# Kernel tuning notes

Measured on AMD Instinct MI355X. Metric: run time of the kernel, lower is better.

Reference implementation:

```python
import jax, jax.numpy as jnp
import numpy as np

DK = 64

def setup_inputs() -> dict:
    key = jax.random.key(0)
    kx, kq, kk, kv = jax.random.split(key, 4)
    B, T, DM, DV = 256, 256, 384, 64
    x = jax.random.normal(kx, (B, T, DM), dtype=jnp.float32)
    s = 1.0 / np.sqrt(DM)
    W_q = jax.random.normal(kq, (DM, DK), dtype=jnp.float32) * s
    W_k = jax.random.normal(kk, (DM, DK), dtype=jnp.float32) * s
    W_v = jax.random.normal(kv, (DM, DV), dtype=jnp.float32) * s
    return {"x": x, "W_q": W_q, "W_k": W_k, "W_v": W_v}

def reference(x, W_q, W_k, W_v):
    # x: [B, T, dm]; projections to [B, T, dk]/[B, T, dv]
    q = jnp.einsum('btc,ck->btk', x, W_q)
    k = jnp.einsum('btc,ck->btk', x, W_k)
    v = jnp.einsum('btc,cv->btv', x, W_v)
    scale = k.shape[-1] ** (-0.5)
    wei = jnp.einsum('btk,bsk->bts', q, k) * scale  # [B, T, T]
    T = x.shape[1]
    causal = jnp.tril(jnp.ones((T, T), dtype=bool))
    wei = jnp.where(causal, wei, -jnp.inf)
    wei = jax.nn.softmax(wei, axis=-1)
    # dropout omitted (eval mode / deterministic reference)
    out = jnp.einsum('bts,bsv->btv', wei, v)
    return out
```

## Files before the change

kernel.cpp:

```cpp
#include <hip/hip_runtime.h>


typedef __attribute__((ext_vector_type(8))) short short8;
typedef __attribute__((ext_vector_type(4))) float floatx4;

__device__ inline unsigned short f2bf(float f) {
  union { float f; unsigned u; } v; v.f = f;
  unsigned r = v.u + 0x7FFFu + ((v.u >> 16) & 1u);
  return (unsigned short)(r >> 16);
}

__device__ inline void glds16(const void* g, void* l) {
  __builtin_amdgcn_global_load_lds(
      (const __attribute__((address_space(1))) void*)g,
      (__attribute__((address_space(3))) void*)l, 16, 0, 0);
}

__global__ void wt_kernel(const float* __restrict__ wq, const float* __restrict__ wk,
                          const float* __restrict__ wv, unsigned short* __restrict__ wt) {
  int idx = blockIdx.x * 256 + threadIdx.x;
  if (idx >= 3 * 64 * 384) return;
  int mat = idx / (64 * 384);
  int rem = idx % (64 * 384);
  int n = rem / 384, k = rem % 384;
  const float* w = (mat == 0) ? wq : ((mat == 1) ? wk : wv);
  wt[idx] = f2bf(w[k * 64 + n]);
}

__global__ __launch_bounds__(1024) void fused_kernel(
    const float* __restrict__ x, const unsigned short* __restrict__ wt,
    float* __restrict__ out) {
  __shared__ __align__(16) unsigned short wb[2][3 * 192 * 32];
  __shared__ __align__(16) unsigned short sK[256 * 72];
  __shared__ __align__(16) unsigned short sVT[64 * 264];

  int tid = threadIdx.x, lane = tid & 63, w = tid >> 6;
  int m = lane & 15, q = lane >> 4;
  int b = blockIdx.x;
  const float* xb = x + (size_t)b * 256 * 384;

  auto stage = [&](int mega, int buf) {
#pragma unroll
    for (int t = 0; t < 3; ++t) {
      int i = w + 16 * t;
      if (i < 36) {
        int kc = i / 12, sub = i % 12;
        int c = sub * 16 + (lane >> 2), g = lane & 3;
        glds16(wt + (size_t)c * 384 + (mega * 3 + kc) * 32 + g * 8,
               (void*)&wb[buf][kc * 6144 + sub * 512]);
      }
    }
  };

  floatx4 z = {0.f, 0.f, 0.f, 0.f};
  floatx4 acc[12];
#pragma unroll
  for (int nt = 0; nt < 12; ++nt) acc[nt] = z;

  stage(0, 0);
#pragma unroll
  for (int mega = 0; mega < 4; ++mega) {
    int buf = mega & 1;
    __syncthreads();
    if (mega < 3) stage(mega + 1, buf ^ 1);

#pragma unroll
    for (int kc = 0; kc < 3; ++kc) {
      int ks = mega * 3 + kc;
      const float* ap = xb + (size_t)(w * 16 + m) * 384 + ks * 32 + q * 8;
      float4 f0 = *(const float4*)ap;
      float4 f1 = *(const float4*)(ap + 4);
      short8 af;
      af[0] = (short)f2bf(f0.x); af[1] = (short)f2bf(f0.y);
      af[2] = (short)f2bf(f0.z); af[3] = (short)f2bf(f0.w);
      af[4] = (short)f2bf(f1.x); af[5] = (short)f2bf(f1.y);
      af[6] = (short)f2bf(f1.z); af[7] = (short)f2bf(f1.w);

      const unsigned short* wbk = &wb[buf][kc * 6144];
#pragma unroll
      for (int nt = 0; nt < 12; ++nt) {
        short8 bf = *(const short8*)&wbk[(nt * 16 + m) * 32 + q * 8];
        acc[nt] = __builtin_amdgcn_mfma_f32_16x16x32_bf16(af, bf, acc[nt], 0, 0, 0);
      }
    }
  }

  unsigned short* scr = &wb[0][0] + w * 1152;
#pragma unroll
  for (int nt = 0; nt < 8; ++nt) {
#pragma unroll
    for (int j = 0; j < 4; ++j) {
      unsigned short val = f2bf(acc[nt][j]);
      int lrow = q * 4 + j;
      if (nt < 4) scr[lrow * 72 + nt * 16 + m] = val;
      else        sK[(w * 16 + lrow) * 72 + (nt - 4) * 16 + m] = val;
    }
  }
#pragma unroll
  for (int nt = 8; nt < 12; ++nt) {
    ushort4 pv;
    pv.x = f2bf(acc[nt][0]); pv.y = f2bf(acc[nt][1]);
    pv.z = f2bf(acc[nt][2]); pv.w = f2bf(acc[nt][3]);
    *(ushort4*)&sVT[((nt - 8) * 16 + m) * 264 + w * 16 + q * 4] = pv;
  }

  short8 qf0 = *(const short8*)(scr + m * 72 + q * 8);
  short8 qf1 = *(const short8*)(scr + m * 72 + 32 + q * 8);

  __syncthreads();

  floatx4 sacc[16];
#pragma unroll
  for (int nt = 0; nt < 16; ++nt) {
    if (nt > w) continue;
    short8 kb0 = *(const short8*)(sK + (nt * 16 + m) * 72 + q * 8);
    short8 kb1 = *(const short8*)(sK + (nt * 16 + m) * 72 + 32 + q * 8);
    floatx4 t = __builtin_amdgcn_mfma_f32_16x16x32_bf16(qf0, kb0, z, 0, 0, 0);
    sacc[nt] = __builtin_amdgcn_mfma_f32_16x16x32_bf16(qf1, kb1, t, 0, 0, 0);
  }

  const float CSC = 0.18033688011112042f;
  float inv_[4];
  int rbase = w * 16 + q * 4;
#pragma unroll
  for (int j = 0; j < 4; ++j) {
    int rg = rbase + j;
    float sum = 0.f;
#pragma unroll
    for (int nt = 0; nt < 16; ++nt) {
      if (nt > w) continue;
      int col = nt * 16 + m;
      float p = (col <= rg) ? exp2f(sacc[nt][j] * CSC) : 0.f;
      sacc[nt][j] = p;
      sum += p;
    }
    sum += __shfl_xor(sum, 1);
    sum += __shfl_xor(sum, 2);
    sum += __shfl_xor(sum, 4);
    sum += __shfl_xor(sum, 8);
    inv_[j] = 1.f / sum;
  }

  floatx4 o[4];
#pragma unroll
  for (int vt = 0; vt < 4; ++vt) o[vt] = z;
#pragma unroll
  for (int c = 0; c < 4; ++c) {
    if (4 * c > w) continue;
#pragma unroll
    for (int t = 0; t < 4; ++t) {
      int nt = 4 * c + t;
#pragma unroll
      for (int j = 0; j < 4; ++j) {
        unsigned short pv = (nt <= w) ? f2bf(sacc[nt][j] * inv_[j]) : (unsigned short)0;
        scr[(q * 4 + j) * 72 + t * 16 + m] = pv;
      }
    }
    short8 pf0 = *(const short8*)(scr + m * 72 + q * 8);
    short8 pf1 = *(const short8*)(scr + m * 72 + 32 + q * 8);
#pragma unroll
    for (int vt = 0; vt < 4; ++vt) {
      short8 vb0 = *(const short8*)(sVT + (vt * 16 + m) * 264 + c * 64 + q * 8);
      short8 vb1 = *(const short8*)(sVT + (vt * 16 + m) * 264 + c * 64 + 32 + q * 8);
      o[vt] = __builtin_amdgcn_mfma_f32_16x16x32_bf16(pf0, vb0, o[vt], 0, 0, 0);
      o[vt] = __builtin_amdgcn_mfma_f32_16x16x32_bf16(pf1, vb1, o[vt], 0, 0, 0);
    }
  }

  float* op = out + ((size_t)b * 256 + w * 16) * 64;
#pragma unroll
  for (int vt = 0; vt < 4; ++vt)
#pragma unroll
    for (int j = 0; j < 4; ++j)
      op[(q * 4 + j) * 64 + vt * 16 + m] = o[vt][j];
}

extern "C" void kernel_launch(void* const* d_in, const int* in_sizes, int n_in,
                              void* d_out, int out_size, void* d_ws, size_t ws_size,
                              hipStream_t stream) {
  const float* x  = (const float*)d_in[0];
  const float* wq = (const float*)d_in[1];
  const float* wk = (const float*)d_in[2];
  const float* wv = (const float*)d_in[3];
  float* out = (float*)d_out;

  unsigned short* wt = (unsigned short*)d_ws;

  wt_kernel<<<288, 256, 0, stream>>>(wq, wk, wv, wt);
  fused_kernel<<<256, 1024, 0, stream>>>(x, wt, out);
}
```

Baseline: 171.4 us.

## Stage x tiles through LDS with async loads and unify shared memory buffer

The projection GEMM now streams x through LDS using global_load_lds, double-buffered alongside the weight tiles, instead of each wave reading x directly from global memory inside the loop. The K loop becomes 12 single-chunk steps with smaller weight stages, and all shared arrays are carved out of one byte buffer that is reused after a new barrier. The aim is to overlap x loads with MFMA work and hide global latency. In exchange it adds 12 block-wide barriers instead of 4 and shorter prefetch distance per step.

```diff
diff --git a/kernel.cpp b/kernel.cpp
--- a/kernel.cpp
+++ b/kernel.cpp
@@ -30,25 +30,22 @@
 __global__ __launch_bounds__(1024) void fused_kernel(
     const float* __restrict__ x, const unsigned short* __restrict__ wt,
     float* __restrict__ out) {
-  __shared__ __align__(16) unsigned short wb[2][3 * 192 * 32];
-  __shared__ __align__(16) unsigned short sK[256 * 72];
-  __shared__ __align__(16) unsigned short sVT[64 * 264];
+  __shared__ __align__(16) unsigned char U[107520];
 
   int tid = threadIdx.x, lane = tid & 63, w = tid >> 6;
   int m = lane & 15, q = lane >> 4;
   int b = blockIdx.x;
   const float* xb = x + (size_t)b * 256 * 384;
 
-  auto stage = [&](int mega, int buf) {
-#pragma unroll
-    for (int t = 0; t < 3; ++t) {
-      int i = w + 16 * t;
-      if (i < 36) {
-        int kc = i / 12, sub = i % 12;
-        int c = sub * 16 + (lane >> 2), g = lane & 3;
-        glds16(wt + (size_t)c * 384 + (mega * 3 + kc) * 32 + g * 8,
-               (void*)&wb[buf][kc * 6144 + sub * 512]);
-      }
+  auto stage = [&](int kc, int buf) {
+    unsigned char* xdst = U + 24576 + buf * 32768 + w * 2048;
+    const float* xsrc = xb + (size_t)(w * 16 + (lane & 15)) * 384 + kc * 32
+                        + ((lane >> 4) * 2) * 4;
+    glds16(xsrc, xdst);
+    glds16(xsrc + 4, xdst + 1024);
+    if (w < 12) {
+      int c = w * 16 + (lane >> 2), g = lane & 3;
+      glds16(wt + (size_t)c * 384 + kc * 32 + g * 8, U + buf * 12288 + w * 1024);
     }
   };
 
@@ -59,33 +56,33 @@
 
   stage(0, 0);
 #pragma unroll
-  for (int mega = 0; mega < 4; ++mega) {
-    int buf = mega & 1;
+  for (int kc = 0; kc < 12; ++kc) {
+    int buf = kc & 1;
     __syncthreads();
-    if (mega < 3) stage(mega + 1, buf ^ 1);
+    if (kc < 11) stage(kc + 1, buf ^ 1);
 
+    const unsigned char* xba = U + 24576 + buf * 32768 + w * 2048 + (16 * q + m) * 16;
+    float4 f0 = *(const float4*)xba;
+    float4 f1 = *(const float4*)(xba + 1024);
+    short8 af;
+    af[0] = (short)f2bf(f0.x); af[1] = (short)f2bf(f0.y);
+    af[2] = (short)f2bf(f0.z); af[3] = (short)f2bf(f0.w);
+    af[4] = (short)f2bf(f1.x); af[5] = (short)f2bf(f1.y);
+    af[6] = (short)f2bf(f1.z); af[7] = (short)f2bf(f1.w);
+
+    const unsigned short* wbk = (const unsigned short*)(U + buf * 12288);
 #pragma unroll
-    for (int kc = 0; kc < 3; ++kc) {
-      int ks = mega * 3 + kc;
-      const float* ap = xb + (size_t)(w * 16 + m) * 384 + ks * 32 + q * 8;
-      float4 f0 = *(const float4*)ap;
-      float4 f1 = *(const float4*)(ap + 4);
-      short8 af;
-      af[0] = (short)f2bf(f0.x); af[1] = (short)f2bf(f0.y);
-      af[2] = (short)f2bf(f0.z); af[3] = (short)f2bf(f0.w);
-      af[4] = (short)f2bf(f1.x); af[5] = (short)f2bf(f1.y);
-      af[6] = (short)f2bf(f1.z); af[7] = (short)f2bf(f1.w);
-
-      const unsigned short* wbk = &wb[buf][kc * 6144];
-#pragma unroll
-      for (int nt = 0; nt < 12; ++nt) {
-        short8 bf = *(const short8*)&wbk[(nt * 16 + m) * 32 + q * 8];
-        acc[nt] = __builtin_amdgcn_mfma_f32_16x16x32_bf16(af, bf, acc[nt], 0, 0, 0);
-      }
+    for (int nt = 0; nt < 12; ++nt) {
+      short8 bf = *(const short8*)&wbk[(nt * 16 + m) * 32 + q * 8];
+      acc[nt] = __builtin_amdgcn_mfma_f32_16x16x32_bf16(af, bf, acc[nt], 0, 0, 0);
     }
   }
 
-  unsigned short* scr = &wb[0][0] + w * 1152;
+  __syncthreads();
+
+  unsigned short* sK  = (unsigned short*)U;
+  unsigned short* sVT = (unsigned short*)(U + 36864);
+  unsigned short* scr = (unsigned short*)(U + 70656) + w * 1152;
 #pragma unroll
   for (int nt = 0; nt < 8; ++nt) {
 #pragma unroll
```

Measured after the change: 174.8 us. Within noise of the previous version (+2.0%).
